# Kernel optimization log

Hardware: AMD Instinct MI355X
Metric: run time of the kernel (lower is better)

Reference implementation:

```python
import jax, jax.numpy as jnp
import numpy as np

B, S, HIDDEN, N_HEADS = 1, 2048, 2048, 16
HEAD_DIM = HIDDEN // N_HEADS  # 128


def setup_inputs() -> dict:
    key = jax.random.key(0)
    ks = jax.random.split(key, 7)
    w = 0.02  # init scale for projection weights
    return {
        "x_self": jax.random.normal(ks[0], (B, S, HIDDEN), jnp.float32),
        "x_cross": jax.random.normal(ks[1], (B, S, HIDDEN), jnp.float32),
        "mask": jnp.zeros((B, 1, S, S), jnp.float32),
        "Wq": jax.random.normal(ks[2], (HIDDEN, HIDDEN), jnp.float32) * w,
        "Wk": jax.random.normal(ks[3], (HIDDEN, HIDDEN), jnp.float32) * w,
        "Wv": jax.random.normal(ks[4], (HIDDEN, HIDDEN), jnp.float32) * w,
        "Wo": jax.random.normal(ks[5], (HIDDEN, HIDDEN), jnp.float32) * w,
    }


def reference(x_self, x_cross, mask, Wq, Wk, Wv, Wo):
    bf16 = jnp.bfloat16
    b = x_self.shape[0]
    scale = HEAD_DIM ** -0.5

    def split_heads(x):  # [b, s, hidden] -> [b, h, s, d]
        return x.reshape(b, -1, N_HEADS, HEAD_DIM).transpose(0, 2, 1, 3)

    # projections run in bf16 (weights cast to bf16 in the original)
    q_self = split_heads((x_self.astype(bf16) @ Wq.astype(bf16).T))
    q_cross = split_heads((x_cross.astype(bf16) @ Wq.astype(bf16).T))
    # k/v for both self and cross blocks come from x_self with identical weights
    k = split_heads((x_self.astype(bf16) @ Wk.astype(bf16).T))
    v = split_heads((x_self.astype(bf16) @ Wv.astype(bf16).T))

    def attn_block(qh):
        # fp32 upcast for QK^T + softmax, then bf16 cast for AV (dropout p=0 -> identity)
        w = jnp.einsum('bhqd,bhkd->bhqk', qh.astype(jnp.float32), k.astype(jnp.float32)) * scale
        w = w + mask
        w = jax.nn.softmax(w, axis=-1).astype(bf16)
        return jnp.einsum('bhqk,bhkd->bhqd', w, v.astype(bf16))  # [b, h, s, d] bf16

    out_self = attn_block(q_self)
    out_cross = attn_block(q_cross)
    out = jnp.concatenate([out_self, out_cross], axis=1)          # [b, 2h, s, d]
    out_flat = out.transpose(0, 2, 1, 3).reshape(b, -1, HIDDEN)   # [b, 2s, hidden]
    Wo_bf = Wo.astype(bf16)
    out_final = 0.5 * (out_flat @ Wo_bf.T + out_flat @ Wo_bf.T)
    return out_final.astype(jnp.float32)
```

## Files before the change

### kernel.cpp

```cpp
#include <hip/hip_runtime.h>
#include <hip/hip_bf16.h>
#include <stdint.h>

#define S 2048
#define HID 2048
#define NH 16
#define HD 128

typedef short short8 __attribute__((ext_vector_type(8)));
typedef float f32x4 __attribute__((ext_vector_type(4)));
typedef float f32x16 __attribute__((ext_vector_type(16)));
typedef uint32_t u32;
typedef u32 u32x4 __attribute__((ext_vector_type(4)));

__device__ __forceinline__ ushort f2bf(float x) {
  uint32_t u = __builtin_bit_cast(uint32_t, x);
  if ((u & 0x7fffffffu) > 0x7f800000u) return (ushort)((u >> 16) | 0x40);
  uint32_t r = u + 0x7fffu + ((u >> 16) & 1u);
  return (ushort)(r >> 16);
}
__device__ __forceinline__ float bf2f(ushort u) {
  union { uint32_t i; float f; } c; c.i = ((uint32_t)u) << 16; return c.f;
}

__device__ __forceinline__ void glds16(const ushort* g, ushort* l) {
  __builtin_amdgcn_global_load_lds((const __attribute__((address_space(1))) uint32_t*)g,
                                   (__attribute__((address_space(3))) uint32_t*)l, 16, 0, 0);
}

__device__ __forceinline__ void mfma16(f32x4& d, short8 a, short8 b) {
  asm volatile("v_mfma_f32_16x16x32_bf16 %0, %1, %2, %0" : "+v"(d) : "v"(a), "v"(b));
}
__device__ __forceinline__ void mfma32(f32x16& d, short8 a, short8 b) {
  asm volatile("v_mfma_f32_32x32x16_bf16 %0, %1, %2, %0" : "+v"(d) : "v"(a), "v"(b));
}
#define MFMA_FENCE() do {                              \
    asm volatile("s_nop 7\n\ts_nop 7\n\ts_nop 7");     \
    __builtin_amdgcn_sched_barrier(0);                 \
  } while (0)
#define RAW_BARRIER() asm volatile("s_barrier" ::: "memory")
#define SCHED_FENCE() __builtin_amdgcn_sched_barrier(0)
#define MAX3(a, b, c) fmaxf(fmaxf((a), (b)), (c))
__device__ __forceinline__ void plswap(u32& a, u32& b) {
  asm volatile("v_permlane32_swap_b32 %0, %1" : "+v"(a), "+v"(b));
}
__device__ __forceinline__ u32 cvtpk(float lo, float hi) {
  u32 r; asm volatile("v_cvt_pk_bf16_f32 %0, %1, %2" : "=v"(r) : "v"(lo), "v"(hi)); return r;
}

struct CastArgs { const float* s[6]; ushort* d[6]; };
__global__ __launch_bounds__(256) void cast6_k(CastArgs a) {
  const float* in = a.s[blockIdx.y];
  ushort* out = a.d[blockIdx.y];
  int i = blockIdx.x * 256 + threadIdx.x;
  float4 v = ((const float4*)in)[i];
  ushort4 o;
  o.x = f2bf(v.x); o.y = f2bf(v.y); o.z = f2bf(v.z); o.w = f2bf(v.w);
  ((ushort4*)out)[i] = o;
}

template <int OUTF32, int NSPLIT>
__global__ __launch_bounds__(256)
void gemm_bt_k(const ushort* __restrict__ A, const ushort* __restrict__ B,
               void* __restrict__ C, int M, int N, int K) {
  __shared__ __align__(16) ushort ldsA[128 * 64];
  __shared__ __align__(16) ushort ldsB[128 * 64];
  const int tid = threadIdx.x, lane = tid & 63, wid = tid >> 6;
  const int g = lane >> 4, c = lane & 15;
  const int wr = wid >> 1, wc = wid & 1;
  const long m0 = (long)blockIdx.y * 128, n0 = (long)blockIdx.x * 128;
  const int srow = lane >> 3, sslot = lane & 7;

  f32x4 acc[4][4] = {};

  for (int k0 = 0; k0 < K; k0 += 64) {
#pragma unroll
    for (int i = 0; i < 4; ++i) {
      int ii = wid * 4 + i;
      int rt = ii * 8 + srow;
      int col = ((sslot ^ (rt & 7)) << 3) + k0;
      glds16(A + (m0 + rt) * (long)K + col, ldsA + ii * 512);
      glds16(B + (n0 + rt) * (long)K + col, ldsB + ii * 512);
    }
    __syncthreads();
#pragma unroll
    for (int kk = 0; kk < 2; ++kk) {
      short8 af[4], bfr[4];
#pragma unroll
      for (int m = 0; m < 4; ++m) {
        int row = wr * 64 + m * 16 + c;
        af[m] = *(const short8*)(ldsA + row * 64 + (((kk * 4 + g) ^ (row & 7)) << 3));
      }
#pragma unroll
      for (int n = 0; n < 4; ++n) {
        int row = wc * 64 + n * 16 + c;
        bfr[n] = *(const short8*)(ldsB + row * 64 + (((kk * 4 + g) ^ (row & 7)) << 3));
      }
#pragma unroll
      for (int m = 0; m < 4; ++m)
#pragma unroll
        for (int n = 0; n < 4; ++n) mfma16(acc[m][n], af[m], bfr[n]);
    }
    __syncthreads();
  }
  MFMA_FENCE();
#pragma unroll
  for (int m = 0; m < 4; ++m) {
#pragma unroll
    for (int r = 0; r < 4; ++r) {
      long grow = m0 + wr * 64 + m * 16 + g * 4 + r;
#pragma unroll
      for (int n = 0; n < 4; ++n) {
        long gcol = n0 + wc * 64 + n * 16 + c;
        long idx;
        if (NSPLIT) idx = ((gcol >> 11) << 22) + (grow << 11) + (gcol & 2047);
        else        idx = grow * N + gcol;
        float v = acc[m][n][r];
        if (OUTF32) ((float*)C)[idx] = bf2f(f2bf(v));
        else        ((ushort*)C)[idx] = f2bf(v);
      }
    }
  }
}

__global__ __launch_bounds__(256)
void transpose_bf16_k(const ushort* __restrict__ in, ushort* __restrict__ out) {
  __shared__ __align__(16) ushort t[64][72];
  const int tid = threadIdx.x;
  const long bx = (long)blockIdx.x * 64;
  const long by = (long)blockIdx.y * 64;
#pragma unroll
  for (int i = 0; i < 2; ++i) {
    int row = (tid >> 3) + i * 32;
    int col = (tid & 7) * 8;
    *(short8*)(&t[row][col]) = *(const short8*)(in + (by + row) * 2048 + bx + col);
  }
  __syncthreads();
#pragma unroll
  for (int i = 0; i < 2; ++i) {
    int orow = (tid >> 3) + i * 32;
    int ocol = (tid & 7) * 8;
    short8 v;
#pragma unroll
    for (int j = 0; j < 8; ++j) v[j] = (short)t[ocol + j][orow];
    *(short8*)(out + (bx + orow) * 2048 + by + ocol) = v;
  }
}

__global__ __launch_bounds__(256)
void maskQ_k(const float* __restrict__ in, ushort* __restrict__ out) {
  __shared__ ushort t[64][72];
  const int tid = threadIdx.x;
  const long q0 = (long)blockIdx.y * 64;
  const long k0 = (long)blockIdx.x * 64;
#pragma unroll
  for (int i = 0; i < 4; ++i) {
    int row = i * 16 + (tid >> 4);
    int col = (tid & 15) * 4;
    float4 v = *(const float4*)(in + (q0 + row) * S + k0 + col);
    t[col + 0][row] = f2bf(v.x);
    t[col + 1][row] = f2bf(v.y);
    t[col + 2][row] = f2bf(v.z);
    t[col + 3][row] = f2bf(v.w);
  }
  __syncthreads();
#pragma unroll
  for (int i = 0; i < 4; ++i) {
    int r4 = i * 4 + (tid >> 6);
    int q = tid & 63;
    ushort4 o;
    o.x = t[r4 * 4 + 0][q];
    o.y = t[r4 * 4 + 1][q];
    o.z = t[r4 * 4 + 2][q];
    o.w = t[r4 * 4 + 3][q];
    *(ushort4*)(out + ((k0 >> 2) + r4) * (S * 4) + (q0 + q) * 4) = o;
  }
}

__global__ __launch_bounds__(256)
void attn7_k(const ushort* __restrict__ Qself, const ushort* __restrict__ Qcross,
             const ushort* __restrict__ Kp, const ushort* __restrict__ Vt,
             const ushort* __restrict__ maskQ, ushort* __restrict__ outf) {
  __shared__ __align__(16) ushort ldsK[2 * 64 * 128];
  __shared__ __align__(16) ushort ldsV[2 * 128 * 64];
  const int tid = threadIdx.x, lane = tid & 63, wid = tid >> 6;
  const int c31 = lane & 31, hi = lane >> 5;

  const int b = blockIdx.x;
  const int xcd = b & 7, j = b >> 3;
  const int h = xcd + 8 * (j & 1);
  const int blk = (j >> 1) & 1;
  const int qt = j >> 2;

  const ushort* Qp = blk ? Qcross : Qself;
  const int qbase = qt * 128 + wid * 32;
  const long qme = qbase + c31;

  short8 qf[8];
#pragma unroll
  for (int ks = 0; ks < 8; ++ks)
    qf[ks] = *(const short8*)(Qp + qme * HID + h * HD + ks * 16 + hi * 8);

  f32x16 o[4] = {};
  float m_r = -__builtin_inff(), l_r = 0.f;

  const float SC  = 0.08838834764831845f;
  const float L2E = 1.4426950408889634f;
  const float THR = 5.545177444479562f;

  const int kRow4 = lane >> 4, kSlot = lane & 15;
  const int vRow8 = lane >> 3, vSlot = lane & 7;
  const ushort* mqp = maskQ + qme * 4 + hi * (S * 4);

#define STAGE(BO, KV0) do {                                                       \
    _Pragma("unroll")                                                             \
    for (int i_ = 0; i_ < 4; ++i_) {                                              \
      int seg = i_ * 4 + wid;                                                     \
      int rk = seg * 4 + kRow4;                                                   \
      glds16(Kp + (long)((KV0) + rk) * HID + h * HD + ((kSlot ^ (rk & 15)) << 3), \
             ldsK + (BO) * 8192 + seg * 512);                                     \
      int rv = seg * 8 + vRow8;                                                   \
      glds16(Vt + (long)(h * HD + rv) * S + (KV0) + ((vSlot ^ (rv & 7)) << 3),    \
             ldsV + (BO) * 8192 + seg * 512);                                     \
    }                                                                             \
  } while (0)

  STAGE(0, 0);

#pragma clang loop unroll(disable)
  for (int t = 0; t < 32; ++t) {
    const int bo = t & 1;
    const ushort* kb = ldsK + bo * 8192;
    const ushort* vb = ldsV + bo * 8192;

    ushort4 mq4[8];
#pragma unroll
    for (int jj = 0; jj < 8; ++jj)
      mq4[jj] = *(const ushort4*)(mqp + ((jj & 3) * 2 + (jj >> 2) * 8) * (S * 4));
    SCHED_FENCE();
    STAGE(bo ^ 1, ((t + 1) & 31) * 64);
    SCHED_FENCE();
    asm volatile("s_waitcnt vmcnt(16)");
    SCHED_FENCE();
    RAW_BARRIER();

    f32x16 s0 = {}, s1 = {};
    __builtin_amdgcn_s_setprio(1);
#pragma unroll
    for (int ks = 0; ks < 8; ++ks) {
      int r0 = c31, r1 = 32 + c31;
      short8 kf0 = *(const short8*)(kb + r0 * 128 + (((ks * 2 + hi) ^ (r0 & 15)) << 3));
      short8 kf1 = *(const short8*)(kb + r1 * 128 + (((ks * 2 + hi) ^ (r1 & 15)) << 3));
      mfma32(s0, kf0, qf[ks]);
      mfma32(s1, kf1, qf[ks]);
    }
    __builtin_amdgcn_s_setprio(0);
    MFMA_FENCE();

#pragma unroll
    for (int r = 0; r < 16; ++r) {
      s0[r] = __builtin_fmaf(s0[r], SC, bf2f(mq4[r >> 2][r & 3]));
      s1[r] = __builtin_fmaf(s1[r], SC, bf2f(mq4[4 + (r >> 2)][r & 3]));
    }

    float a0 = MAX3(s0[0], s0[1], s0[2]);
    float a1 = MAX3(s0[3], s0[4], s0[5]);
    float a2 = MAX3(s0[6], s0[7], s0[8]);
    float a3 = MAX3(s0[9], s0[10], s0[11]);
    float a4 = MAX3(s0[12], s0[13], s0[14]);
    float a5 = MAX3(s0[15], s1[0], s1[1]);
    float a6 = MAX3(s1[2], s1[3], s1[4]);
    float a7 = MAX3(s1[5], s1[6], s1[7]);
    float a8 = MAX3(s1[8], s1[9], s1[10]);
    float a9 = MAX3(s1[11], s1[12], s1[13]);
    float a10 = fmaxf(s1[14], s1[15]);
    float b0 = MAX3(a0, a1, a2);
    float b1 = MAX3(a3, a4, a5);
    float b2 = MAX3(a6, a7, a8);
    float b3 = fmaxf(a9, a10);
    float pm = MAX3(b0, b1, fmaxf(b2, b3));
    float pmax = fmaxf(pm, __shfl_xor(pm, 32));

    if (!__all(pmax <= m_r + THR)) {
      float mnew = fmaxf(m_r, pmax);
      float alpha = __builtin_amdgcn_exp2f((m_r - mnew) * L2E);
      m_r = mnew;
      l_r *= alpha;
#pragma unroll
      for (int r = 0; r < 16; ++r) {
        float alf = __shfl(alpha, (r & 3) + 8 * (r >> 2) + 4 * hi);
#pragma unroll
        for (int dt = 0; dt < 4; ++dt) o[dt][r] *= alf;
      }
    }

    const float nm = -m_r * L2E;
#pragma unroll
    for (int r = 0; r < 16; ++r) {
      s0[r] = __builtin_amdgcn_exp2f(__builtin_fmaf(s0[r], L2E, nm));
      s1[r] = __builtin_amdgcn_exp2f(__builtin_fmaf(s1[r], L2E, nm));
    }
    float sm[16];
#pragma unroll
    for (int r = 0; r < 16; ++r) sm[r] = s0[r] + s1[r];
#pragma unroll
    for (int st = 8; st >= 1; st >>= 1)
#pragma unroll
      for (int i = 0; i < 8; ++i)
        if (i < st) sm[i] += sm[i + st];
    l_r += sm[0] + __shfl_xor(sm[0], 32);

    short8 pa[4];
#pragma unroll
    for (int kk = 0; kk < 4; ++kk) {
      const f32x16& sv = (kk < 2) ? s0 : s1;
      const int bq = (kk & 1) * 8;
      u32 x0 = cvtpk(sv[bq + 0], sv[bq + 1]);
      u32 x1 = cvtpk(sv[bq + 2], sv[bq + 3]);
      u32 y0 = cvtpk(sv[bq + 4], sv[bq + 5]);
      u32 y1 = cvtpk(sv[bq + 6], sv[bq + 7]);
      plswap(x0, y0);
      plswap(x1, y1);
      u32x4 tt; tt[0] = x0; tt[1] = x1; tt[2] = y0; tt[3] = y1;
      pa[kk] = __builtin_bit_cast(short8, tt);
    }
    asm volatile("s_nop 1");
    SCHED_FENCE();

    __builtin_amdgcn_s_setprio(1);
#pragma unroll
    for (int kk = 0; kk < 4; ++kk) {
#pragma unroll
      for (int dt = 0; dt < 4; ++dt) {
        int row = dt * 32 + c31;
        short8 vf = *(const short8*)(vb + row * 64 + (((kk * 2 + hi) ^ (row & 7)) << 3));
        mfma32(o[dt], pa[kk], vf);
      }
    }
    __builtin_amdgcn_s_setprio(0);

    RAW_BARRIER();
    mqp += 16 * (S * 4);
  }
#undef STAGE

  MFMA_FENCE();
#pragma unroll
  for (int r = 0; r < 16; ++r) {
    int qr = (r & 3) + 8 * (r >> 2) + 4 * hi;
    float linv = 1.0f / __shfl(l_r, qr);
    long orow = 2L * (qbase + qr) + blk;
#pragma unroll
    for (int dt = 0; dt < 4; ++dt)
      outf[orow * HID + h * HD + dt * 32 + c31] = f2bf(o[dt][r] * linv);
  }
}

extern "C" void kernel_launch(void* const* d_in, const int* in_sizes, int n_in,
                              void* d_out, int out_size, void* d_ws, size_t ws_size,
                              hipStream_t stream) {
  (void)in_sizes; (void)n_in; (void)out_size; (void)ws_size;
  const float* x_self  = (const float*)d_in[0];
  const float* x_cross = (const float*)d_in[1];
  const float* mask    = (const float*)d_in[2];
  const float* Wq      = (const float*)d_in[3];
  const float* Wk      = (const float*)d_in[4];
  const float* Wv      = (const float*)d_in[5];
  const float* Wo      = (const float*)d_in[6];

  uint8_t* w = (uint8_t*)d_ws;
  const size_t MB8 = (size_t)S * HID * sizeof(ushort);
  ushort* xs_bf   = (ushort*)(w + 0 * MB8);
  ushort* xc_bf   = (ushort*)(w + 1 * MB8);
  ushort* Wq_bf   = (ushort*)(w + 2 * MB8);
  ushort* Wk_bf   = (ushort*)(w + 3 * MB8);
  ushort* Wv_bf   = (ushort*)(w + 4 * MB8);
  ushort* Wo_bf   = (ushort*)(w + 5 * MB8);
  ushort* q_self  = (ushort*)(w + 6 * MB8);
  ushort* q_cross = (ushort*)(w + 7 * MB8);
  ushort* k_      = (ushort*)(w + 8 * MB8);
  ushort* v_      = (ushort*)(w + 9 * MB8);
  ushort* vt       = xs_bf;
  ushort* out_flat = Wq_bf;
  ushort* maskQ    = v_;

  CastArgs ca;
  ca.s[0] = x_self;  ca.d[0] = xs_bf;
  ca.s[1] = x_cross; ca.d[1] = xc_bf;
  ca.s[2] = Wq;      ca.d[2] = Wq_bf;
  ca.s[3] = Wk;      ca.d[3] = Wk_bf;
  ca.s[4] = Wv;      ca.d[4] = Wv_bf;
  ca.s[5] = Wo;      ca.d[5] = Wo_bf;
  cast6_k<<<dim3(4096, 6), 256, 0, stream>>>(ca);

  gemm_bt_k<0, 0><<<dim3(16, 32), 256, 0, stream>>>(xs_bf, Wq_bf, q_self, 4096, 2048, 2048);
  gemm_bt_k<0, 1><<<dim3(32, 16), 256, 0, stream>>>(xs_bf, Wk_bf, k_, 2048, 4096, 2048);

  transpose_bf16_k<<<dim3(32, 32), 256, 0, stream>>>(v_, vt);
  maskQ_k<<<dim3(32, 32), 256, 0, stream>>>(mask, maskQ);

  attn7_k<<<dim3(512), 256, 0, stream>>>(q_self, q_cross, k_, vt, maskQ, out_flat);

  gemm_bt_k<1, 0><<<dim3(16, 32), 256, 0, stream>>>(out_flat, Wo_bf, d_out, 4096, 2048, 2048);
}
```

Before: 245.8 us.

## Software-pipeline attention QK with PV across iterations and merge Q/KV GEMM launches

The attention loop is restructured so that QK^T for the next KV tile is issued while softmax and PV for the current tile run, using double-buffered score registers and mask prefetch. K is staged two tiles ahead and V one tile ahead. The Q and K/V projection GEMMs are also merged into a single launch with 1024 blocks, and the output GEMM is given a 1D grid. This is meant to overlap MFMA work with the softmax VALU work and cut launch overhead, at the cost of higher register pressure and more complex barrier and waitcnt bookkeeping.

```diff
diff --git a/kernel.cpp b/kernel.cpp
--- a/kernel.cpp
+++ b/kernel.cpp
@@ -60,15 +60,14 @@
 }
 
 template <int OUTF32, int NSPLIT>
-__global__ __launch_bounds__(256)
-void gemm_bt_k(const ushort* __restrict__ A, const ushort* __restrict__ B,
-               void* __restrict__ C, int M, int N, int K) {
-  __shared__ __align__(16) ushort ldsA[128 * 64];
-  __shared__ __align__(16) ushort ldsB[128 * 64];
+__device__ __forceinline__ void gemm_tile(const ushort* __restrict__ A,
+                                          const ushort* __restrict__ B,
+                                          void* __restrict__ C, int N, int K,
+                                          int bx, int by, ushort* ldsA, ushort* ldsB) {
   const int tid = threadIdx.x, lane = tid & 63, wid = tid >> 6;
   const int g = lane >> 4, c = lane & 15;
   const int wr = wid >> 1, wc = wid & 1;
-  const long m0 = (long)blockIdx.y * 128, n0 = (long)blockIdx.x * 128;
+  const long m0 = (long)by * 128, n0 = (long)bx * 128;
   const int srow = lane >> 3, sslot = lane & 7;
 
   f32x4 acc[4][4] = {};
@@ -124,6 +123,29 @@
 }
 
 __global__ __launch_bounds__(256)
+void gemm_qkv_k(const ushort* __restrict__ xs, const ushort* __restrict__ Wq,
+                ushort* __restrict__ q, const ushort* __restrict__ Wkv,
+                ushort* __restrict__ kv) {
+  __shared__ __align__(16) ushort ldsA[128 * 64];
+  __shared__ __align__(16) ushort ldsB[128 * 64];
+  const int bid = blockIdx.x;
+  if (bid < 512) {
+    gemm_tile<0, 0>(xs, Wq, q, 2048, 2048, bid & 15, bid >> 4, ldsA, ldsB);
+  } else {
+    const int b2 = bid - 512;
+    gemm_tile<0, 1>(xs, Wkv, kv, 4096, 2048, b2 & 31, b2 >> 5, ldsA, ldsB);
+  }
+}
+
+__global__ __launch_bounds__(256)
+void gemm_out_k(const ushort* __restrict__ A, const ushort* __restrict__ B,
+                float* __restrict__ C) {
+  __shared__ __align__(16) ushort ldsA[128 * 64];
+  __shared__ __align__(16) ushort ldsB[128 * 64];
+  gemm_tile<1, 0>(A, B, C, 2048, 2048, blockIdx.x & 15, blockIdx.x >> 4, ldsA, ldsB);
+}
+
+__global__ __launch_bounds__(256)
 void transpose_bf16_k(const ushort* __restrict__ in, ushort* __restrict__ out) {
   __shared__ __align__(16) ushort t[64][72];
   const int tid = threadIdx.x;
@@ -178,7 +200,7 @@
 }
 
 __global__ __launch_bounds__(256)
-void attn7_k(const ushort* __restrict__ Qself, const ushort* __restrict__ Qcross,
+void attn8_k(const ushort* __restrict__ Qself, const ushort* __restrict__ Qcross,
              const ushort* __restrict__ Kp, const ushort* __restrict__ Vt,
              const ushort* __restrict__ maskQ, ushort* __restrict__ outf) {
   __shared__ __align__(16) ushort ldsK[2 * 64 * 128];
@@ -202,6 +224,8 @@
     qf[ks] = *(const short8*)(Qp + qme * HID + h * HD + ks * 16 + hi * 8);
 
   f32x16 o[4] = {};
+  f32x16 sA0, sA1, sB0, sB1;
+  ushort4 mqA[8], mqB[8];
   float m_r = -__builtin_inff(), l_r = 0.f;
 
   const float SC  = 0.08838834764831845f;
@@ -212,137 +236,164 @@
   const int vRow8 = lane >> 3, vSlot = lane & 7;
   const ushort* mqp = maskQ + qme * 4 + hi * (S * 4);
 
-#define STAGE(BO, KV0) do {                                                       \
+#define STAGE_K(BO, KV0) do {                                                     \
     _Pragma("unroll")                                                             \
     for (int i_ = 0; i_ < 4; ++i_) {                                              \
       int seg = i_ * 4 + wid;                                                     \
       int rk = seg * 4 + kRow4;                                                   \
       glds16(Kp + (long)((KV0) + rk) * HID + h * HD + ((kSlot ^ (rk & 15)) << 3), \
              ldsK + (BO) * 8192 + seg * 512);                                     \
+    } } while (0)
+
+#define STAGE_V(BO, KV0) do {                                                     \
+    _Pragma("unroll")                                                             \
+    for (int i_ = 0; i_ < 4; ++i_) {                                              \
+      int seg = i_ * 4 + wid;                                                     \
       int rv = seg * 8 + vRow8;                                                   \
       glds16(Vt + (long)(h * HD + rv) * S + (KV0) + ((vSlot ^ (rv & 7)) << 3),    \
              ldsV + (BO) * 8192 + seg * 512);                                     \
+    } } while (0)
+
+#define LOAD_MASKS(DST, T) do {                                                   \
+    const long mrow_ = (long)(((T)) & 31) * 16;                                   \
+    _Pragma("unroll")                                                             \
+    for (int jj = 0; jj < 8; ++jj)                                                \
+      (DST)[jj] = *(const ushort4*)(mqp + (mrow_ + (jj & 3) * 2 + (jj >> 2) * 8) * (S * 4)); \
+  } while (0)
+
+#define QK_CLUSTER(S0W, S1W, P) do {                                              \
+    const ushort* kb_ = ldsK + ((P) ^ 1) * 8192;                                  \
+    _Pragma("unroll")                                                             \
+    for (int r_ = 0; r_ < 16; ++r_) { (S0W)[r_] = 0.f; (S1W)[r_] = 0.f; }         \
+    _Pragma("unroll")                                                             \
+    for (int ks = 0; ks < 8; ++ks) {                                              \
+      short8 kf0 = *(const short8*)(kb_ + c31 * 128 + (((ks * 2 + hi) ^ (c31 & 15)) << 3)); \
+      short8 kf1 = *(const short8*)(kb_ + (32 + c31) * 128 + (((ks * 2 + hi) ^ ((32 + c31) & 15)) << 3)); \
+      mfma32((S0W), kf0, qf[ks]);                                                 \
+      mfma32((S1W), kf1, qf[ks]);                                                 \
+    } } while (0)
+
+#define BODY(T, P, S0R, S1R, S0W, S1W, MRD, MWR) do {                             \
+    SCHED_FENCE();    \
+    LOAD_MASKS(MWR, (T) + 1);                                                     \
+    SCHED_FENCE();                                                                \
+    STAGE_V((P) ^ 1, (((T) + 1) & 31) * 64);                                      \
+    STAGE_K((P), (((T) + 2) & 31) * 64);                                          \
+    SCHED_FENCE();                                                                \
+    asm volatile("s_waitcnt vmcnt(16)");                                          \
+    SCHED_FENCE();                                                                \
+    RAW_BARRIER();                                                                \
+           \
+    QK_CLUSTER(S0W, S1W, P);                                                      \
+    _Pragma("unroll")                                                             \
+    for (int r = 0; r < 16; ++r) {                                                \
+      (S0R)[r] = __builtin_fmaf((S0R)[r], SC, bf2f((MRD)[r >> 2][r & 3]));        \
+      (S1R)[r] = __builtin_fmaf((S1R)[r], SC, bf2f((MRD)[4 + (r >> 2)][r & 3]));  \
     }                                                                             \
+    {                                                                             \
+      float a0 = MAX3((S0R)[0], (S0R)[1], (S0R)[2]);                              \
+      float a1 = MAX3((S0R)[3], (S0R)[4], (S0R)[5]);                              \
+      float a2 = MAX3((S0R)[6], (S0R)[7], (S0R)[8]);                              \
+      float a3 = MAX3((S0R)[9], (S0R)[10], (S0R)[11]);                            \
+      float a4 = MAX3((S0R)[12], (S0R)[13], (S0R)[14]);                           \
+      float a5 = MAX3((S0R)[15], (S1R)[0], (S1R)[1]);                             \
+      float a6 = MAX3((S1R)[2], (S1R)[3], (S1R)[4]);                              \
+      float a7 = MAX3((S1R)[5], (S1R)[6], (S1R)[7]);                              \
+      float a8 = MAX3((S1R)[8], (S1R)[9], (S1R)[10]);                             \
+      float a9 = MAX3((S1R)[11], (S1R)[12], (S1R)[13]);                           \
+      float a10 = fmaxf((S1R)[14], (S1R)[15]);                                    \
+      float b0 = MAX3(a0, a1, a2);                                                \
+      float b1 = MAX3(a3, a4, a5);                                                \
+      float b2 = MAX3(a6, a7, a8);                                                \
+      float b3 = fmaxf(a9, a10);                                                  \
+      float pm = MAX3(b0, b1, fmaxf(b2, b3));                                     \
+      float pmax = fmaxf(pm, __shfl_xor(pm, 32));                                 \
+      if (!__all(pmax <= m_r + THR)) {                                            \
+        float mnew = fmaxf(m_r, pmax);                                            \
+        float alpha = __builtin_amdgcn_exp2f((m_r - mnew) * L2E);                 \
+        m_r = mnew;                                                               \
+        l_r *= alpha;                                                             \
+        _Pragma("unroll")                                                         \
+        for (int r = 0; r < 16; ++r) {                                            \
+          float alf = __shfl(alpha, (r & 3) + 8 * (r >> 2) + 4 * hi);             \
+          _Pragma("unroll")                                                       \
+          for (int dt = 0; dt < 4; ++dt) o[dt][r] *= alf;                         \
+        }                                                                         \
+      }                                                                           \
+    }                                                                             \
+    {                                                                             \
+      const float nm = -m_r * L2E;                                                \
+      _Pragma("unroll")                                                           \
+      for (int r = 0; r < 16; ++r) {                                              \
+        (S0R)[r] = __builtin_amdgcn_exp2f(__builtin_fmaf((S0R)[r], L2E, nm));     \
+        (S1R)[r] = __builtin_amdgcn_exp2f(__builtin_fmaf((S1R)[r], L2E, nm));     \
+      }                                                                           \
+      float sm[16];                                                               \
+      _Pragma("unroll")                                                           \
+      for (int r = 0; r < 16; ++r) sm[r] = (S0R)[r] + (S1R)[r];                   \
+      _Pragma("unroll")                                                           \
+      for (int st = 8; st >= 1; st >>= 1)                                         \
+        _Pragma("unroll")                                                         \
+        for (int i = 0; i < 8; ++i)                                               \
+          if (i < st) sm[i] += sm[i + st];                                        \
+      l_r += sm[0] + __shfl_xor(sm[0], 32);                                       \
+    }                                                                             \
+    short8 pa[4];                                                                 \
+    _Pragma("unroll")                                                             \
+    for (int kk = 0; kk < 4; ++kk) {                                              \
+      const f32x16& sv = (kk < 2) ? (S0R) : (S1R);                                \
+      const int bq = (kk & 1) * 8;                                                \
+      u32 x0 = cvtpk(sv[bq + 0], sv[bq + 1]);                                     \
+      u32 x1 = cvtpk(sv[bq + 2], sv[bq + 3]);                                     \
+      u32 y0 = cvtpk(sv[bq + 4], sv[bq + 5]);                                     \
+      u32 y1 = cvtpk(sv[bq + 6], sv[bq + 7]);                                     \
+      plswap(x0, y0);                                                             \
+      plswap(x1, y1);                                                             \
+      u32x4 tt; tt[0] = x0; tt[1] = x1; tt[2] = y0; tt[3] = y1;                   \
+      pa[kk] = __builtin_bit_cast(short8, tt);                                    \
+    }                                                                             \
+    asm volatile("s_nop 1");                                                      \
+    SCHED_FENCE();                                                                \
+    {                                                                             \
+      const ushort* vb_ = ldsV + (P) * 8192;                                      \
+      __builtin_amdgcn_s_setprio(1);                                              \
+      _Pragma("unroll")                                                           \
+      for (int kk = 0; kk < 4; ++kk) {                                            \
+        _Pragma("unroll")                                                         \
+        for (int dt = 0; dt < 4; ++dt) {                                          \
+          int row = dt * 32 + c31;                                                \
+          short8 vf = *(const short8*)(vb_ + row * 64 + (((kk * 2 + hi) ^ (row & 7)) << 3)); \
+          mfma32(o[dt], pa[kk], vf);                                              \
+        }                                                                         \
+      }                                                                           \
+      __builtin_amdgcn_s_setprio(0);                                              \
+    }                                                                             \
+    RAW_BARRIER();                                                                \
   } while (0)
 
-  STAGE(0, 0);
+  LOAD_MASKS(mqA, 0);
+  SCHED_FENCE();
+  STAGE_V(0, 0);
+  STAGE_K(0, 0);
+  STAGE_K(1, 64);
+  SCHED_FENCE();
+  asm volatile("s_waitcnt vmcnt(4)");
+  SCHED_FENCE();
+  RAW_BARRIER();
+  QK_CLUSTER(sA0, sA1, 1);
+  MFMA_FENCE();
+  RAW_BARRIER();
 
 #pragma clang loop unroll(disable)
-  for (int t = 0; t < 32; ++t) {
-    const int bo = t & 1;
-    const ushort* kb = ldsK + bo * 8192;
-    const ushort* vb = ldsV + bo * 8192;
-
-    ushort4 mq4[8];
-#pragma unroll
-    for (int jj = 0; jj < 8; ++jj)
-      mq4[jj] = *(const ushort4*)(mqp + ((jj & 3) * 2 + (jj >> 2) * 8) * (S * 4));
-    SCHED_FENCE();
-    STAGE(bo ^ 1, ((t + 1) & 31) * 64);
-    SCHED_FENCE();
-    asm volatile("s_waitcnt vmcnt(16)");
-    SCHED_FENCE();
-    RAW_BARRIER();
-
-    f32x16 s0 = {}, s1 = {};
-    __builtin_amdgcn_s_setprio(1);
-#pragma unroll
-    for (int ks = 0; ks < 8; ++ks) {
-      int r0 = c31, r1 = 32 + c31;
-      short8 kf0 = *(const short8*)(kb + r0 * 128 + (((ks * 2 + hi) ^ (r0 & 15)) << 3));
-      short8 kf1 = *(const short8*)(kb + r1 * 128 + (((ks * 2 + hi) ^ (r1 & 15)) << 3));
-      mfma32(s0, kf0, qf[ks]);
-      mfma32(s1, kf1, qf[ks]);
-    }
-    __builtin_amdgcn_s_setprio(0);
-    MFMA_FENCE();
-
-#pragma unroll
-    for (int r = 0; r < 16; ++r) {
-      s0[r] = __builtin_fmaf(s0[r], SC, bf2f(mq4[r >> 2][r & 3]));
-      s1[r] = __builtin_fmaf(s1[r], SC, bf2f(mq4[4 + (r >> 2)][r & 3]));
-    }
-
-    float a0 = MAX3(s0[0], s0[1], s0[2]);
-    float a1 = MAX3(s0[3], s0[4], s0[5]);
-    float a2 = MAX3(s0[6], s0[7], s0[8]);
-    float a3 = MAX3(s0[9], s0[10], s0[11]);
-    float a4 = MAX3(s0[12], s0[13], s0[14]);
-    float a5 = MAX3(s0[15], s1[0], s1[1]);
-    float a6 = MAX3(s1[2], s1[3], s1[4]);
-    float a7 = MAX3(s1[5], s1[6], s1[7]);
-    float a8 = MAX3(s1[8], s1[9], s1[10]);
-    float a9 = MAX3(s1[11], s1[12], s1[13]);
-    float a10 = fmaxf(s1[14], s1[15]);
-    float b0 = MAX3(a0, a1, a2);
-    float b1 = MAX3(a3, a4, a5);
-    float b2 = MAX3(a6, a7, a8);
-    float b3 = fmaxf(a9, a10);
-    float pm = MAX3(b0, b1, fmaxf(b2, b3));
-    float pmax = fmaxf(pm, __shfl_xor(pm, 32));
-
-    if (!__all(pmax <= m_r + THR)) {
-      float mnew = fmaxf(m_r, pmax);
-      float alpha = __builtin_amdgcn_exp2f((m_r - mnew) * L2E);
-      m_r = mnew;
-      l_r *= alpha;
-#pragma unroll
-      for (int r = 0; r < 16; ++r) {
-        float alf = __shfl(alpha, (r & 3) + 8 * (r >> 2) + 4 * hi);
-#pragma unroll
-        for (int dt = 0; dt < 4; ++dt) o[dt][r] *= alf;
-      }
-    }
-
-    const float nm = -m_r * L2E;
-#pragma unroll
-    for (int r = 0; r < 16; ++r) {
-      s0[r] = __builtin_amdgcn_exp2f(__builtin_fmaf(s0[r], L2E, nm));
-      s1[r] = __builtin_amdgcn_exp2f(__builtin_fmaf(s1[r], L2E, nm));
-    }
-    float sm[16];
-#pragma unroll
-    for (int r = 0; r < 16; ++r) sm[r] = s0[r] + s1[r];
-#pragma unroll
-    for (int st = 8; st >= 1; st >>= 1)
-#pragma unroll
-      for (int i = 0; i < 8; ++i)
-        if (i < st) sm[i] += sm[i + st];
-    l_r += sm[0] + __shfl_xor(sm[0], 32);
-
-    short8 pa[4];
-#pragma unroll
-    for (int kk = 0; kk < 4; ++kk) {
-      const f32x16& sv = (kk < 2) ? s0 : s1;
-      const int bq = (kk & 1) * 8;
-      u32 x0 = cvtpk(sv[bq + 0], sv[bq + 1]);
-      u32 x1 = cvtpk(sv[bq + 2], sv[bq + 3]);
-      u32 y0 = cvtpk(sv[bq + 4], sv[bq + 5]);
-      u32 y1 = cvtpk(sv[bq + 6], sv[bq + 7]);
-      plswap(x0, y0);
-      plswap(x1, y1);
-      u32x4 tt; tt[0] = x0; tt[1] = x1; tt[2] = y0; tt[3] = y1;
-      pa[kk] = __builtin_bit_cast(short8, tt);
-    }
-    asm volatile("s_nop 1");
-    SCHED_FENCE();
-
-    __builtin_amdgcn_s_setprio(1);
-#pragma unroll
-    for (int kk = 0; kk < 4; ++kk) {
-#pragma unroll
-      for (int dt = 0; dt < 4; ++dt) {
-        int row = dt * 32 + c31;
-        short8 vf = *(const short8*)(vb + row * 64 + (((kk * 2 + hi) ^ (row & 7)) << 3));
-        mfma32(o[dt], pa[kk], vf);
-      }
-    }
-    __builtin_amdgcn_s_setprio(0);
-
-    RAW_BARRIER();
-    mqp += 16 * (S * 4);
-  }
-#undef STAGE
+  for (int t = 0; t < 32; t += 2) {
+    BODY(t,     0, sA0, sA1, sB0, sB1, mqA, mqB);
+    BODY(t + 1, 1, sB0, sB1, sA0, sA1, mqB, mqA);
+  }
+#undef BODY
+#undef QK_CLUSTER
+#undef LOAD_MASKS
+#undef STAGE_V
+#undef STAGE_K
 
   MFMA_FENCE();
 #pragma unroll
@@ -393,13 +444,12 @@
   ca.s[5] = Wo;      ca.d[5] = Wo_bf;
   cast6_k<<<dim3(4096, 6), 256, 0, stream>>>(ca);
 
-  gemm_bt_k<0, 0><<<dim3(16, 32), 256, 0, stream>>>(xs_bf, Wq_bf, q_self, 4096, 2048, 2048);
-  gemm_bt_k<0, 1><<<dim3(32, 16), 256, 0, stream>>>(xs_bf, Wk_bf, k_, 2048, 4096, 2048);
+  gemm_qkv_k<<<dim3(1024), 256, 0, stream>>>(xs_bf, Wq_bf, q_self, Wk_bf, k_);
 
   transpose_bf16_k<<<dim3(32, 32), 256, 0, stream>>>(v_, vt);
   maskQ_k<<<dim3(32, 32), 256, 0, stream>>>(mask, maskQ);
 
-  attn7_k<<<dim3(512), 256, 0, stream>>>(q_self, q_cross, k_, vt, maskQ, out_flat);
-
-  gemm_bt_k<1, 0><<<dim3(16, 32), 256, 0, stream>>>(out_flat, Wo_bf, d_out, 4096, 2048, 2048);
-}
+  attn8_k<<<dim3(512), 256, 0, stream>>>(q_self, q_cross, k_, vt, maskQ, out_flat);
+
+  gemm_out_k<<<dim3(512), 256, 0, stream>>>(out_flat, Wo_bf, (float*)d_out);
+}
```

Measured after the change: 302.5 us. 23.1% more time.

## Fuse fp32-to-bf16 weight cast into GEMM B-tile loads; zero-init first MFMA

Applied to the files above, without the earlier changes.

Weights are no longer pre-cast by a separate kernel. Each GEMM now reads fp32 weight rows directly, converts them to bf16 with packed converts, and writes them into LDS, replacing the async global-to-LDS load for B. This removes four 8 MB bf16 weight writes and their re-reads, but doubles the B-side global traffic per tile and uses synchronous register-staged loads, which may stall the GEMM main loop. The attention kernel's first QK MFMA also uses a zero accumulator instead of zero-initialising registers.

```diff
diff --git a/kernel.cpp b/kernel.cpp
--- a/kernel.cpp
+++ b/kernel.cpp
@@ -33,6 +33,11 @@
 }
 __device__ __forceinline__ void mfma32(f32x16& d, short8 a, short8 b) {
   asm volatile("v_mfma_f32_32x32x16_bf16 %0, %1, %2, %0" : "+v"(d) : "v"(a), "v"(b));
+}
+__device__ __forceinline__ f32x16 mfma32_z(short8 a, short8 b) {
+  f32x16 d;
+  asm volatile("v_mfma_f32_32x32x16_bf16 %0, %1, %2, 0" : "=v"(d) : "v"(a), "v"(b));
+  return d;
 }
 #define MFMA_FENCE() do {                              \
     asm volatile("s_nop 7\n\ts_nop 7\n\ts_nop 7");     \
@@ -48,8 +53,8 @@
   u32 r; asm volatile("v_cvt_pk_bf16_f32 %0, %1, %2" : "=v"(r) : "v"(lo), "v"(hi)); return r;
 }
 
-struct CastArgs { const float* s[6]; ushort* d[6]; };
-__global__ __launch_bounds__(256) void cast6_k(CastArgs a) {
+struct CastArgs { const float* s[2]; ushort* d[2]; };
+__global__ __launch_bounds__(256) void cast2_k(CastArgs a) {
   const float* in = a.s[blockIdx.y];
   ushort* out = a.d[blockIdx.y];
   int i = blockIdx.x * 256 + threadIdx.x;
@@ -61,8 +66,9 @@
 
 template <int OUTF32, int NSPLIT>
 __global__ __launch_bounds__(256)
-void gemm_bt_k(const ushort* __restrict__ A, const ushort* __restrict__ B,
-               void* __restrict__ C, int M, int N, int K) {
+void gemm_bt_k(const ushort* __restrict__ A, const float* __restrict__ Bf,
+               const float* __restrict__ Bf2, void* __restrict__ C,
+               int M, int N, int K) {
   __shared__ __align__(16) ushort ldsA[128 * 64];
   __shared__ __align__(16) ushort ldsB[128 * 64];
   const int tid = threadIdx.x, lane = tid & 63, wid = tid >> 6;
@@ -71,6 +77,9 @@
   const long m0 = (long)blockIdx.y * 128, n0 = (long)blockIdx.x * 128;
   const int srow = lane >> 3, sslot = lane & 7;
 
+  const float* Bbase = (!NSPLIT || n0 < 2048) ? Bf : Bf2;
+  const long nb = (!NSPLIT || n0 < 2048) ? n0 : n0 - 2048;
+
   f32x4 acc[4][4] = {};
 
   for (int k0 = 0; k0 < K; k0 += 64) {
@@ -80,7 +89,15 @@
       int rt = ii * 8 + srow;
       int col = ((sslot ^ (rt & 7)) << 3) + k0;
       glds16(A + (m0 + rt) * (long)K + col, ldsA + ii * 512);
-      glds16(B + (n0 + rt) * (long)K + col, ldsB + ii * 512);
+      const float* bp = Bbase + (nb + rt) * (long)K + col;
+      float4 x0 = *(const float4*)bp;
+      float4 x1 = *(const float4*)(bp + 4);
+      u32x4 pk;
+      pk[0] = cvtpk(x0.x, x0.y);
+      pk[1] = cvtpk(x0.z, x0.w);
+      pk[2] = cvtpk(x1.x, x1.y);
+      pk[3] = cvtpk(x1.z, x1.w);
+      *(u32x4*)(ldsB + ii * 512 + lane * 8) = pk;
     }
     __syncthreads();
 #pragma unroll
@@ -244,10 +261,17 @@
     SCHED_FENCE();
     RAW_BARRIER();
 
-    f32x16 s0 = {}, s1 = {};
+    f32x16 s0, s1;
     __builtin_amdgcn_s_setprio(1);
-#pragma unroll
-    for (int ks = 0; ks < 8; ++ks) {
+    {
+      const int r0 = c31, r1 = 32 + c31;
+      short8 kf0 = *(const short8*)(kb + r0 * 128 + ((hi ^ (r0 & 15)) << 3));
+      short8 kf1 = *(const short8*)(kb + r1 * 128 + ((hi ^ (r1 & 15)) << 3));
+      s0 = mfma32_z(kf0, qf[0]);
+      s1 = mfma32_z(kf1, qf[0]);
+    }
+#pragma unroll
+    for (int ks = 1; ks < 8; ++ks) {
       int r0 = c31, r1 = 32 + c31;
       short8 kf0 = *(const short8*)(kb + r0 * 128 + (((ks * 2 + hi) ^ (r0 & 15)) << 3));
       short8 kf1 = *(const short8*)(kb + r1 * 128 + (((ks * 2 + hi) ^ (r1 & 15)) << 3));
@@ -370,36 +394,31 @@
 
   uint8_t* w = (uint8_t*)d_ws;
   const size_t MB8 = (size_t)S * HID * sizeof(ushort);
-  ushort* xs_bf   = (ushort*)(w + 0 * MB8);
-  ushort* xc_bf   = (ushort*)(w + 1 * MB8);
-  ushort* Wq_bf   = (ushort*)(w + 2 * MB8);
-  ushort* Wk_bf   = (ushort*)(w + 3 * MB8);
-  ushort* Wv_bf   = (ushort*)(w + 4 * MB8);
-  ushort* Wo_bf   = (ushort*)(w + 5 * MB8);
-  ushort* q_self  = (ushort*)(w + 6 * MB8);
-  ushort* q_cross = (ushort*)(w + 7 * MB8);
-  ushort* k_      = (ushort*)(w + 8 * MB8);
-  ushort* v_      = (ushort*)(w + 9 * MB8);
+  ushort* xs_bf    = (ushort*)(w + 0 * MB8);
+  ushort* xc_bf    = (ushort*)(w + 1 * MB8);
+  ushort* out_flat = (ushort*)(w + 2 * MB8);
+  ushort* q_self   = (ushort*)(w + 4 * MB8);
+  ushort* q_cross  = (ushort*)(w + 5 * MB8);
+  ushort* k_       = (ushort*)(w + 6 * MB8);
+  ushort* v_       = (ushort*)(w + 7 * MB8);
   ushort* vt       = xs_bf;
-  ushort* out_flat = Wq_bf;
   ushort* maskQ    = v_;
 
   CastArgs ca;
   ca.s[0] = x_self;  ca.d[0] = xs_bf;
   ca.s[1] = x_cross; ca.d[1] = xc_bf;
-  ca.s[2] = Wq;      ca.d[2] = Wq_bf;
-  ca.s[3] = Wk;      ca.d[3] = Wk_bf;
-  ca.s[4] = Wv;      ca.d[4] = Wv_bf;
-  ca.s[5] = Wo;      ca.d[5] = Wo_bf;
-  cast6_k<<<dim3(4096, 6), 256, 0, stream>>>(ca);
-
-  gemm_bt_k<0, 0><<<dim3(16, 32), 256, 0, stream>>>(xs_bf, Wq_bf, q_self, 4096, 2048, 2048);
-  gemm_bt_k<0, 1><<<dim3(32, 16), 256, 0, stream>>>(xs_bf, Wk_bf, k_, 2048, 4096, 2048);
+  cast2_k<<<dim3(4096, 2), 256, 0, stream>>>(ca);
+
+  gemm_bt_k<0, 0><<<dim3(16, 32), 256, 0, stream>>>(xs_bf, Wq, nullptr, q_self,
+                                                    4096, 2048, 2048);
+  gemm_bt_k<0, 1><<<dim3(32, 16), 256, 0, stream>>>(xs_bf, Wk, Wv, k_,
+                                                    2048, 4096, 2048);
 
   transpose_bf16_k<<<dim3(32, 32), 256, 0, stream>>>(v_, vt);
   maskQ_k<<<dim3(32, 32), 256, 0, stream>>>(mask, maskQ);
 
   attn7_k<<<dim3(512), 256, 0, stream>>>(q_self, q_cross, k_, vt, maskQ, out_flat);
 
-  gemm_bt_k<1, 0><<<dim3(16, 32), 256, 0, stream>>>(out_flat, Wo_bf, d_out, 4096, 2048, 2048);
-}
+  gemm_bt_k<1, 0><<<dim3(16, 32), 256, 0, stream>>>(out_flat, Wo, nullptr, d_out,
+                                                    4096, 2048, 2048);
+}
```

After: 308.6 us. 25.6% more time.

## Fuse Q and KV projections into one 256x256-tile double-buffered GEMM launch

Applied to the files above, without the earlier changes.

Replaces the two separate 128x128-tile projection GEMM launches with a single kernel of 256 blocks of 512 threads. Each block computes a 256x256 output tile and double-buffers its 64-wide K slices in LDS, prefetching the next slice while the current one is consumed. The goal is more operand reuse per LDS load, overlap of global loads with MFMA work, and one less launch. It also initialises the attention QK^T accumulator with a zero-operand MFMA instead of explicit clearing. The cost is about 128KB of LDS per block, which allows only one block per CU and leaves little latency hiding; any imbalance between the Q and KV halves also shows up directly.

```diff
diff --git a/kernel.cpp b/kernel.cpp
--- a/kernel.cpp
+++ b/kernel.cpp
@@ -33,6 +33,11 @@
 }
 __device__ __forceinline__ void mfma32(f32x16& d, short8 a, short8 b) {
   asm volatile("v_mfma_f32_32x32x16_bf16 %0, %1, %2, %0" : "+v"(d) : "v"(a), "v"(b));
+}
+__device__ __forceinline__ f32x16 mfma32_z(short8 a, short8 b) {
+  f32x16 d;
+  asm volatile("v_mfma_f32_32x32x16_bf16 %0, %1, %2, 0" : "=v"(d) : "v"(a), "v"(b));
+  return d;
 }
 #define MFMA_FENCE() do {                              \
     asm volatile("s_nop 7\n\ts_nop 7\n\ts_nop 7");     \
@@ -57,6 +62,99 @@
   ushort4 o;
   o.x = f2bf(v.x); o.y = f2bf(v.y); o.z = f2bf(v.z); o.w = f2bf(v.w);
   ((ushort4*)out)[i] = o;
+}
+
+template <int OUTF32, int NSPLIT>
+__device__ __forceinline__ void gemm256_body(const ushort* __restrict__ A,
+                                             const ushort* __restrict__ B,
+                                             void* __restrict__ C, int N, int K,
+                                             long m0, long n0,
+                                             ushort* ldsA, ushort* ldsB) {
+  const int tid = threadIdx.x, lane = tid & 63, wid = tid >> 6;
+  const int g = lane >> 4, c = lane & 15;
+  const int wr = wid >> 2, wc = wid & 3;
+  const int srow = lane >> 3, sslot = lane & 7;
+
+  f32x4 acc[8][4] = {};
+
+#define GSTAGE256(BO, K0) do {                                                \
+    _Pragma("unroll")                                                         \
+    for (int i_ = 0; i_ < 4; ++i_) {                                          \
+      int ii = wid * 4 + i_;                \
+      int rt = ii * 8 + srow;                                                 \
+      int col = ((sslot ^ (rt & 7)) << 3) + (K0);                             \
+      glds16(A + (m0 + rt) * (long)K + col, ldsA + (BO) * 16384 + ii * 512);  \
+      glds16(B + (n0 + rt) * (long)K + col, ldsB + (BO) * 16384 + ii * 512);  \
+    } } while (0)
+
+  GSTAGE256(0, 0);
+
+#pragma clang loop unroll(disable)
+  for (int k0 = 0; k0 < K; k0 += 64) {
+    const int bo = (k0 >> 6) & 1;
+    GSTAGE256(bo ^ 1, (k0 + 64 < K) ? (k0 + 64) : 0);
+    SCHED_FENCE();
+    asm volatile("s_waitcnt vmcnt(8)");
+    SCHED_FENCE();
+    RAW_BARRIER();
+    const ushort* la = ldsA + bo * 16384;
+    const ushort* lb = ldsB + bo * 16384;
+#pragma unroll
+    for (int kk = 0; kk < 2; ++kk) {
+      short8 af[8], bfr[4];
+#pragma unroll
+      for (int m = 0; m < 8; ++m) {
+        int row = wr * 128 + m * 16 + c;
+        af[m] = *(const short8*)(la + row * 64 + (((kk * 4 + g) ^ (row & 7)) << 3));
+      }
+#pragma unroll
+      for (int n = 0; n < 4; ++n) {
+        int row = wc * 64 + n * 16 + c;
+        bfr[n] = *(const short8*)(lb + row * 64 + (((kk * 4 + g) ^ (row & 7)) << 3));
+      }
+#pragma unroll
+      for (int m = 0; m < 8; ++m)
+#pragma unroll
+        for (int n = 0; n < 4; ++n) mfma16(acc[m][n], af[m], bfr[n]);
+    }
+    RAW_BARRIER();
+  }
+#undef GSTAGE256
+  MFMA_FENCE();
+#pragma unroll
+  for (int m = 0; m < 8; ++m) {
+#pragma unroll
+    for (int r = 0; r < 4; ++r) {
+      long grow = m0 + wr * 128 + m * 16 + g * 4 + r;
+#pragma unroll
+      for (int n = 0; n < 4; ++n) {
+        long gcol = n0 + wc * 64 + n * 16 + c;
+        long idx;
+        if (NSPLIT) idx = ((gcol >> 11) << 22) + (grow << 11) + (gcol & 2047);
+        else        idx = grow * N + gcol;
+        float v = acc[m][n][r];
+        if (OUTF32) ((float*)C)[idx] = bf2f(f2bf(v));
+        else        ((ushort*)C)[idx] = f2bf(v);
+      }
+    }
+  }
+}
+
+__global__ __launch_bounds__(512)
+void gemm_qkv256_k(const ushort* __restrict__ xs, const ushort* __restrict__ Wq,
+                   ushort* __restrict__ q, const ushort* __restrict__ Wkv,
+                   ushort* __restrict__ kv) {
+  __shared__ __align__(16) ushort ldsA[2 * 256 * 64];
+  __shared__ __align__(16) ushort ldsB[2 * 256 * 64];
+  const int bid = blockIdx.x;
+  if (bid < 128) {
+    gemm256_body<0, 0>(xs, Wq, q, 2048, 2048,
+                       (long)(bid >> 3) * 256, (long)(bid & 7) * 256, ldsA, ldsB);
+  } else {
+    const int b2 = bid - 128;
+    gemm256_body<0, 1>(xs, Wkv, kv, 4096, 2048,
+                       (long)(b2 >> 4) * 256, (long)(b2 & 15) * 256, ldsA, ldsB);
+  }
 }
 
 template <int OUTF32, int NSPLIT>
@@ -244,10 +342,17 @@
     SCHED_FENCE();
     RAW_BARRIER();
 
-    f32x16 s0 = {}, s1 = {};
+    f32x16 s0, s1;
     __builtin_amdgcn_s_setprio(1);
-#pragma unroll
-    for (int ks = 0; ks < 8; ++ks) {
+    {
+      const int r0 = c31, r1 = 32 + c31;
+      short8 kf0 = *(const short8*)(kb + r0 * 128 + ((hi ^ (r0 & 15)) << 3));
+      short8 kf1 = *(const short8*)(kb + r1 * 128 + ((hi ^ (r1 & 15)) << 3));
+      s0 = mfma32_z(kf0, qf[0]);
+      s1 = mfma32_z(kf1, qf[0]);
+    }
+#pragma unroll
+    for (int ks = 1; ks < 8; ++ks) {
       int r0 = c31, r1 = 32 + c31;
       short8 kf0 = *(const short8*)(kb + r0 * 128 + (((ks * 2 + hi) ^ (r0 & 15)) << 3));
       short8 kf1 = *(const short8*)(kb + r1 * 128 + (((ks * 2 + hi) ^ (r1 & 15)) << 3));
@@ -393,8 +498,7 @@
   ca.s[5] = Wo;      ca.d[5] = Wo_bf;
   cast6_k<<<dim3(4096, 6), 256, 0, stream>>>(ca);
 
-  gemm_bt_k<0, 0><<<dim3(16, 32), 256, 0, stream>>>(xs_bf, Wq_bf, q_self, 4096, 2048, 2048);
-  gemm_bt_k<0, 1><<<dim3(32, 16), 256, 0, stream>>>(xs_bf, Wk_bf, k_, 2048, 4096, 2048);
+  gemm_qkv256_k<<<dim3(256), 512, 0, stream>>>(xs_bf, Wq_bf, q_self, Wk_bf, k_);
 
   transpose_bf16_k<<<dim3(32, 32), 256, 0, stream>>>(v_, vt);
   maskQ_k<<<dim3(32, 32), 256, 0, stream>>>(mask, maskQ);
```

Measured after the change: 237.1 us. 3.5% less time.
